# Kernel optimization log

Measured on AMD Instinct MI355X. Metric: run time of the kernel, lower is better.

Reference implementation:

```python
import jax, jax.numpy as jnp
import numpy as np

B, D, H, NG = 8192, 2048, 2048, 7  # batch, input_size, hidden_size, num gate networks


def setup_inputs() -> dict:
    key = jax.random.key(0)
    ks = jax.random.split(key, 7)
    hx = jax.random.normal(ks[0], (B, D), dtype=jnp.float32)
    cx1 = jax.random.normal(ks[1], (B, H), dtype=jnp.float32)
    cx2 = jax.random.normal(ks[2], (B, H), dtype=jnp.float32)
    tj = jax.random.uniform(ks[3], (B, 1), dtype=jnp.float32)
    dt = jax.random.uniform(ks[4], (B, 1), dtype=jnp.float32)
    # fused weights for the 7 gate/decay networks, order: i1,i2,f1,f2,o,z,d
    W = jax.random.normal(ks[5], (D, NG * H), dtype=jnp.float32) * (1.0 / np.sqrt(D))
    b = jax.random.normal(ks[6], (NG * H,), dtype=jnp.float32) * 0.01
    return {"hx": hx, "cx1": cx1, "cx2": cx2, "tj": tj, "dt": dt, "W": W, "b": b}


def reference(hx, cx1, cx2, tj, dt, W, b):
    # One fused GEMM for all 7 gate networks, then split.
    g = hx @ W + b  # [B, 7H]
    i1, i2, f1, f2, o, z_raw, d_raw = [g[:, k * H:(k + 1) * H] for k in range(NG)]
    sig = jax.nn.sigmoid
    i1, i2, f1, f2, o = sig(i1), sig(i2), sig(f1), sig(f2), sig(o)
    z = jnp.tanh(z_raw)                 # Tanh(LC_z(hx)) as in forward
    decay = jax.nn.softplus(d_raw)      # Decay_network: positive decay coeff
    cy1 = f1 * cx1 + i1 * z             # fast cell state
    cy2 = f2 * cx2 + i2 * z             # asymptotic cell state
    t = tj + dt
    # continuous-time decay: c(t) = cy2 + (cy1 - cy2) * exp(-decay * (t - tj))
    c_t = cy2 + (cy1 - cy2) * jnp.exp(-decay * (t - tj))
    h_t = o * jnp.tanh(c_t)             # get_h(t)
    return jnp.stack([cy1, cy2, h_t])   # [3, B, H]
```

## Files before the change

kernel.cpp:

```cpp
#include <hip/hip_runtime.h>
#include <hip/hip_bf16.h>
#include <stdint.h>


#define B_SZ 8192
#define D_SZ 2048
#define H_SZ 2048
#define NG   7
#define NW   (NG * H_SZ)
#define BM   256
#define BN   32
#define BK   32
#define NKST (D_SZ / BK)
#define NBX  (B_SZ / BM)
#define NBY  (H_SZ / BN)

#define WB_BYTES   ((size_t)NBY * NKST * 14336)
#define HXB_OFF    WB_BYTES
#define HXB_BYTES  ((size_t)NBX * NKST * 16384)
#define WS_NEEDED  (WB_BYTES + HXB_BYTES)

typedef __attribute__((ext_vector_type(8))) short bf16x8;
typedef __attribute__((ext_vector_type(4))) float f32x4;

__device__ __forceinline__ uint32_t cvtpk(float lo, float hi) {
    uint32_t r;
    asm("v_cvt_pk_bf16_f32 %0, %1, %2" : "=v"(r) : "v"(lo), "v"(hi));
    return r;
}
__device__ __forceinline__ void glds16(const void* g, void* l) {
    __builtin_amdgcn_global_load_lds(
        (const __attribute__((address_space(1))) uint32_t*)g,
        (__attribute__((address_space(3))) uint32_t*)l, 16, 0, 0);
}
__device__ __forceinline__ float sigmoidf_(float x) {
    return 1.0f / (1.0f + __expf(-x));
}
__device__ __forceinline__ float tanhf_(float x) {
    float ax = fabsf(x);
    float e = __expf(2.0f * ax);
    float t = 1.0f - 2.0f / (e + 1.0f);
    return copysignf(t, x);
}
__device__ __forceinline__ float softplusf_(float x) {
    return (x > 30.0f) ? x : __logf(1.0f + __expf(x));
}

__global__ __launch_bounds__(896) void conv_w(const float* __restrict__ W,
                                              char* __restrict__ wb)
{
    const int by = blockIdx.x >> 6;
    const int ks = blockIdx.x & 63;
    const int u  = threadIdx.x;
    const int r  = u >> 2;
    const int pc = u & 3;
    const int koct = pc ^ ((r >> 1) & 3);
    const int g  = r >> 5;
    const int n  = r & 31;
    const int col = g * H_SZ + by * BN + n;
    const float* src = W + (size_t)(ks * BK + koct * 8) * NW + col;
    float w0 = src[0];
    float w1 = src[(size_t)NW];
    float w2 = src[(size_t)2 * NW];
    float w3 = src[(size_t)3 * NW];
    float w4 = src[(size_t)4 * NW];
    float w5 = src[(size_t)5 * NW];
    float w6 = src[(size_t)6 * NW];
    float w7 = src[(size_t)7 * NW];
    uint4 o;
    o.x = cvtpk(w0, w1); o.y = cvtpk(w2, w3);
    o.z = cvtpk(w4, w5); o.w = cvtpk(w6, w7);
    *(uint4*)(wb + (size_t)blockIdx.x * 14336 + u * 16) = o;
}

__global__ __launch_bounds__(1024) void conv_hx(const float* __restrict__ hx,
                                                char* __restrict__ hxb)
{
    const int bx = blockIdx.x >> 6;
    const int ks = blockIdx.x & 63;
    const int u  = threadIdx.x;
    const int r  = u >> 2;
    const int pc = u & 3;
    const int koct = pc ^ ((r >> 1) & 3);
    const float* src = hx + (size_t)(bx * BM + r) * D_SZ + ks * BK + koct * 8;
    f32x4 a = *(const f32x4*)(src);
    f32x4 b = *(const f32x4*)(src + 4);
    uint4 o;
    o.x = cvtpk(a[0], a[1]); o.y = cvtpk(a[2], a[3]);
    o.z = cvtpk(b[0], b[1]); o.w = cvtpk(b[2], b[3]);
    *(uint4*)(hxb + (size_t)blockIdx.x * 16384 + u * 16) = o;
}

#define NTH3 512
#define BUFB 30720

#define SB0 __builtin_amdgcn_sched_barrier(0)

__global__ __launch_bounds__(NTH3, 2) void lstm_bf16(
    const char* __restrict__ wb, const char* __restrict__ hxb,
    const float* __restrict__ cx1, const float* __restrict__ cx2,
    const float* __restrict__ dt, const float* __restrict__ bias,
    float* __restrict__ out)
{
    __shared__ char smem[4 * BUFB];

    const int tid  = threadIdx.x;
    const int lane = tid & 63;
    const int wid  = tid >> 6;
    const int wm   = wid >> 1;
    const int wn   = wid & 1;
    const int l15  = lane & 15;
    const int lg   = lane >> 4;

    const int b0  = blockIdx.x;
    const int swz = (b0 & 7) * 256 + (b0 >> 3);
    const int by2 = swz >> 6;
    const int rem = swz & 63;
    const int bx  = rem >> 1;
    const int by  = by2 * 2 + (rem & 1);
    const int gm0 = bx * BM;
    const int n0  = by * BN;

    const int xch = (lg ^ ((l15 >> 1) & 3)) * 8;
    const uint32_t aAb = (uint32_t)(uintptr_t)smem + 2u * ((wm * 64 + l15) * 32 + xch);
    const uint32_t aBb = (uint32_t)(uintptr_t)smem + 16384u + 2u * ((wn * 16 + l15) * 32 + xch);
    const uint32_t aA0 = aAb,            aA1 = aAb + BUFB;
    const uint32_t aA2 = aAb + 2 * BUFB, aA3 = aAb + 3 * BUFB;
    const uint32_t aB0 = aBb,            aB1 = aBb + BUFB;
    const uint32_t aB2 = aBb + 2 * BUFB, aB3 = aBb + 3 * BUFB;

    const int lane16 = lane << 4;
    const char* hxp0 = hxb + (((size_t)(bx * NKST)) << 14) + (wid << 11) + lane16;
    const char* wbp0 = wb + (size_t)(by * NKST) * 14336 + wid * 1792 + lane16;
    char* dA0 = smem + (wid << 11);            char* dB0 = smem + 16384 + wid * 1792;
    char* dA1 = dA0 + BUFB;                    char* dB1 = dB0 + BUFB;
    char* dA2 = dA0 + 2 * BUFB;                char* dB2 = dB0 + 2 * BUFB;
    char* dA3 = dA0 + 3 * BUFB;                char* dB3 = dB0 + 3 * BUFB;

    f32x4 acc[NG][4];
    #pragma unroll
    for (int g = 0; g < NG; ++g)
        #pragma unroll
        for (int mf = 0; mf < 4; ++mf)
            acc[g][mf] = (f32x4){0.f, 0.f, 0.f, 0.f};

    bf16x8 fBE[NG], fBO[NG];
    bf16x8 fA0E, fA0O, fA1, fA2, fA3;

    #define ISSUE_A123(AAc) do {                                                   \
        asm volatile("ds_read_b128 %0, %1 offset:1024" : "=&v"(fA1) : "v"(AAc));   \
        asm volatile("ds_read_b128 %0, %1 offset:2048" : "=&v"(fA2) : "v"(AAc));   \
        asm volatile("ds_read_b128 %0, %1 offset:3072" : "=&v"(fA3) : "v"(AAc));   \
    } while (0)

    #define ISSUE_NEXT(ABn, AAn, FBN, FA0N) do {                                   \
        asm volatile("ds_read_b128 %0, %1"               : "=&v"(FBN[0]) : "v"(ABn)); \
        asm volatile("ds_read_b128 %0, %1 offset:2048"   : "=&v"(FBN[1]) : "v"(ABn)); \
        asm volatile("ds_read_b128 %0, %1 offset:4096"   : "=&v"(FBN[2]) : "v"(ABn)); \
        asm volatile("ds_read_b128 %0, %1 offset:6144"   : "=&v"(FBN[3]) : "v"(ABn)); \
        asm volatile("ds_read_b128 %0, %1 offset:8192"   : "=&v"(FBN[4]) : "v"(ABn)); \
        asm volatile("ds_read_b128 %0, %1 offset:10240"  : "=&v"(FBN[5]) : "v"(ABn)); \
        asm volatile("ds_read_b128 %0, %1 offset:12288"  : "=&v"(FBN[6]) : "v"(ABn)); \
        asm volatile("ds_read_b128 %0, %1"               : "=&v"(FA0N)   : "v"(AAn)); \
    } while (0)

    #define CLUSTER(FA, FBC, MF, LGN) do {                                         \
        asm volatile("s_waitcnt lgkmcnt(" #LGN ")" ::: "memory");                  \
        SB0;                                                                       \
        __builtin_amdgcn_s_setprio(1);                                             \
        _Pragma("unroll")                                                          \
        for (int g_ = 0; g_ < NG; ++g_)                                            \
            acc[g_][MF] = __builtin_amdgcn_mfma_f32_16x16x32_bf16(                 \
                FA, FBC[g_], acc[g_][MF], 0, 0, 0);                                \
        __builtin_amdgcn_s_setprio(0);                                             \
        SB0;                                                                       \
    } while (0)

    #define STAGE(SC) do {                                                         \
        glds16(hxp, dA##SC); glds16(hxp + 1024, dA##SC + 1024);                    \
        glds16(wbp, dB##SC);                                                       \
        if (lane < 48) glds16(wbp + 1024, dB##SC + 1024);                          \
        hxp += 16384; wbp += 14336;                                                \
    } while (0)

    #define STAGE_K(SC, K) do {                                                    \
        glds16(hxp0 + (K) * 16384, dA##SC);                                        \
        glds16(hxp0 + (K) * 16384 + 1024, dA##SC + 1024);                          \
        glds16(wbp0 + (K) * 14336, dB##SC);                                        \
        if (lane < 48) glds16(wbp0 + (K) * 14336 + 1024, dB##SC + 1024);           \
    } while (0)

    #define STEP_S(AAc, ABn, AAn, FBC, FBN, FA0C, FA0N, SC, VMN)  do {             \
        asm volatile("s_waitcnt vmcnt(" #VMN ")" ::: "memory");                    \
        __builtin_amdgcn_s_barrier();                                              \
        SB0;                                                                       \
        ISSUE_A123(AAc);                                                           \
        ISSUE_NEXT(ABn, AAn, FBN, FA0N);                                           \
        SB0;                                                                       \
        STAGE(SC);                                                                 \
        SB0;                                                                       \
        CLUSTER(FA0C, FBC, 0, 11);                                                 \
        CLUSTER(fA1,  FBC, 1, 10);                                                 \
        CLUSTER(fA2,  FBC, 2, 9);                                                  \
        CLUSTER(fA3,  FBC, 3, 8);                                                  \
    } while (0)

    #define STEP_N(AAc, ABn, AAn, FBC, FBN, FA0C, FA0N, VMN)  do {                 \
        asm volatile("s_waitcnt vmcnt(" #VMN ")" ::: "memory");                    \
        __builtin_amdgcn_s_barrier();                                              \
        SB0;                                                                       \
        ISSUE_A123(AAc);                                                           \
        ISSUE_NEXT(ABn, AAn, FBN, FA0N);                                           \
        SB0;                                                                       \
        CLUSTER(FA0C, FBC, 0, 11);                                                 \
        CLUSTER(fA1,  FBC, 1, 10);                                                 \
        CLUSTER(fA2,  FBC, 2, 9);                                                  \
        CLUSTER(fA3,  FBC, 3, 8);                                                  \
    } while (0)

    STAGE_K(0, 0);
    STAGE_K(1, 1);
    STAGE_K(2, 2);
    const char* hxp = hxp0 + 3 * 16384;
    const char* wbp = wbp0 + 3 * 14336;
    asm volatile("s_waitcnt vmcnt(8)" ::: "memory");
    __builtin_amdgcn_s_barrier();
    SB0;
    ISSUE_NEXT(aB0, aA0, fBE, fA0E);
    SB0;

    #pragma unroll 1
    for (int it = 0; it < 15; ++it) {
        STEP_S(aA0, aB1, aA1, fBE, fBO, fA0E, fA0O, 3, 4);
        STEP_S(aA1, aB2, aA2, fBO, fBE, fA0O, fA0E, 0, 4);
        STEP_S(aA2, aB3, aA3, fBE, fBO, fA0E, fA0O, 1, 4);
        STEP_S(aA3, aB0, aA0, fBO, fBE, fA0O, fA0E, 2, 4);
    }
    STEP_S(aA0, aB1, aA1, fBE, fBO, fA0E, fA0O, 3, 4);
    STEP_N(aA1, aB2, aA2, fBO, fBE, fA0O, fA0E, 4);
    STEP_N(aA2, aB3, aA3, fBE, fBO, fA0E, fA0O, 0);
    ISSUE_A123(aA3);
    SB0;
    CLUSTER(fA0O, fBO, 0, 3);
    CLUSTER(fA1,  fBO, 1, 2);
    CLUSTER(fA2,  fBO, 2, 1);
    CLUSTER(fA3,  fBO, 3, 0);

    const size_t BH = (size_t)B_SZ * H_SZ;
    const int j = n0 + wn * 16 + l15;
    float bj[NG];
    #pragma unroll
    for (int g = 0; g < NG; ++g) bj[g] = bias[g * H_SZ + j];

    #pragma unroll
    for (int mf = 0; mf < 4; ++mf) {
        #pragma unroll
        for (int r = 0; r < 4; ++r) {
            int row = gm0 + wm * 64 + mf * 16 + lg * 4 + r;
            float dtv = dt[row];
            float i1 = sigmoidf_(acc[0][mf][r] + bj[0]);
            float i2 = sigmoidf_(acc[1][mf][r] + bj[1]);
            float f1 = sigmoidf_(acc[2][mf][r] + bj[2]);
            float f2 = sigmoidf_(acc[3][mf][r] + bj[3]);
            float o  = sigmoidf_(acc[4][mf][r] + bj[4]);
            float z  = tanhf_(acc[5][mf][r] + bj[5]);
            float dec = softplusf_(acc[6][mf][r] + bj[6]);
            size_t idx = (size_t)row * H_SZ + j;
            float c1 = cx1[idx], c2 = cx2[idx];
            float cy1 = f1 * c1 + i1 * z;
            float cy2 = f2 * c2 + i2 * z;
            float ct  = cy2 + (cy1 - cy2) * __expf(-dec * dtv);
            float ht  = o * tanhf_(ct);
            out[idx]          = cy1;
            out[BH + idx]     = cy2;
            out[2 * BH + idx] = ht;
        }
    }
}

#define NTH  512
#define LDP  40
__global__ __launch_bounds__(NTH, 2) void lstm_f32(
    const float* __restrict__ hx, const float* __restrict__ cx1,
    const float* __restrict__ cx2, const float* __restrict__ dt,
    const float* __restrict__ W, const float* __restrict__ bias,
    float* __restrict__ out)
{
    __shared__ ushort sA[BM * LDP];
    __shared__ ushort sB[NG * BN * LDP];

    const int tid = threadIdx.x;
    const int nwg = gridDim.x;
    const int cpx = nwg >> 3;
    const int b0  = blockIdx.x;
    const int swz = (b0 & 7) * cpx + (b0 >> 3);
    const int bx  = swz & 31;
    const int by  = swz >> 5;
    const int gm0 = bx * BM;
    const int n0  = by * BN;

    const int lane = tid & 63;
    const int wid  = tid >> 6;
    const int wm   = wid >> 1;
    const int wn   = wid & 1;
    const int l15  = lane & 15;
    const int lg   = lane >> 4;

    const int ar0 = tid >> 2,          aq0 = tid & 3;
    const int ar1 = (tid + 512) >> 2,  aq1 = tid & 3;
    const bool hasB = (tid < 448);
    const int bg  = tid >> 6;
    const int bkq = (tid >> 3) & 7;
    const int bnq = tid & 7;

    f32x4 pa[4];
    f32x4 pb[4];

    auto issue_loads = [&](int K0) {
        {
            const float* p = hx + (size_t)(gm0 + ar0) * D_SZ + K0 + aq0 * 8;
            pa[0] = *(const f32x4*)(p);
            pa[1] = *(const f32x4*)(p + 4);
        }
        {
            const float* p = hx + (size_t)(gm0 + ar1) * D_SZ + K0 + aq1 * 8;
            pa[2] = *(const f32x4*)(p);
            pa[3] = *(const f32x4*)(p + 4);
        }
        if (hasB) {
            const float* p = W + (size_t)(K0 + bkq * 4) * NW + bg * H_SZ + n0 + bnq * 4;
            pb[0] = *(const f32x4*)(p);
            pb[1] = *(const f32x4*)(p + NW);
            pb[2] = *(const f32x4*)(p + 2 * NW);
            pb[3] = *(const f32x4*)(p + 3 * NW);
        }
    };

    auto store_lds = [&]() {
        {
            uint4 u;
            u.x = cvtpk(pa[0][0], pa[0][1]); u.y = cvtpk(pa[0][2], pa[0][3]);
            u.z = cvtpk(pa[1][0], pa[1][1]); u.w = cvtpk(pa[1][2], pa[1][3]);
            *(uint4*)(&sA[ar0 * LDP + aq0 * 8]) = u;
        }
        {
            uint4 u;
            u.x = cvtpk(pa[2][0], pa[2][1]); u.y = cvtpk(pa[2][2], pa[2][3]);
            u.z = cvtpk(pa[3][0], pa[3][1]); u.w = cvtpk(pa[3][2], pa[3][3]);
            *(uint4*)(&sA[ar1 * LDP + aq1 * 8]) = u;
        }
        if (hasB) {
            #pragma unroll
            for (int jj = 0; jj < 4; ++jj) {
                uint2 v;
                v.x = cvtpk(pb[0][jj], pb[1][jj]);
                v.y = cvtpk(pb[2][jj], pb[3][jj]);
                *(uint2*)(&sB[(bg * BN + bnq * 4 + jj) * LDP + bkq * 4]) = v;
            }
        }
    };

    f32x4 acc[NG][4];
    #pragma unroll
    for (int g = 0; g < NG; ++g)
        #pragma unroll
        for (int mf = 0; mf < 4; ++mf)
            acc[g][mf] = (f32x4){0.f, 0.f, 0.f, 0.f};

    int aoff[4];
    #pragma unroll
    for (int mf = 0; mf < 4; ++mf)
        aoff[mf] = (wm * 64 + mf * 16 + l15) * LDP + lg * 8;
    int boff[NG];
    #pragma unroll
    for (int g = 0; g < NG; ++g)
        boff[g] = (g * BN + wn * 16 + l15) * LDP + lg * 8;

    issue_loads(0);
    for (int kk = 0; kk < NKST; ++kk) {
        store_lds();
        __syncthreads();
        if (kk + 1 < NKST) issue_loads((kk + 1) * BK);

        bf16x8 af[4];
        #pragma unroll
        for (int mf = 0; mf < 4; ++mf)
            af[mf] = *(const bf16x8*)(&sA[aoff[mf]]);
        #pragma unroll
        for (int g = 0; g < NG; ++g) {
            bf16x8 bfr = *(const bf16x8*)(&sB[boff[g]]);
            #pragma unroll
            for (int mf = 0; mf < 4; ++mf)
                acc[g][mf] = __builtin_amdgcn_mfma_f32_16x16x32_bf16(
                    af[mf], bfr, acc[g][mf], 0, 0, 0);
        }
        __syncthreads();
    }

    const size_t BH = (size_t)B_SZ * H_SZ;
    const int j = n0 + wn * 16 + l15;
    float bj[NG];
    #pragma unroll
    for (int g = 0; g < NG; ++g) bj[g] = bias[g * H_SZ + j];

    #pragma unroll
    for (int mf = 0; mf < 4; ++mf) {
        #pragma unroll
        for (int r = 0; r < 4; ++r) {
            int row = gm0 + wm * 64 + mf * 16 + lg * 4 + r;
            float dtv = dt[row];
            float i1 = sigmoidf_(acc[0][mf][r] + bj[0]);
            float i2 = sigmoidf_(acc[1][mf][r] + bj[1]);
            float f1 = sigmoidf_(acc[2][mf][r] + bj[2]);
            float f2 = sigmoidf_(acc[3][mf][r] + bj[3]);
            float o  = sigmoidf_(acc[4][mf][r] + bj[4]);
            float z  = tanhf_(acc[5][mf][r] + bj[5]);
            float dec = softplusf_(acc[6][mf][r] + bj[6]);
            size_t idx = (size_t)row * H_SZ + j;
            float c1 = cx1[idx], c2 = cx2[idx];
            float cy1 = f1 * c1 + i1 * z;
            float cy2 = f2 * c2 + i2 * z;
            float ct  = cy2 + (cy1 - cy2) * __expf(-dec * dtv);
            float ht  = o * tanhf_(ct);
            out[idx]          = cy1;
            out[BH + idx]     = cy2;
            out[2 * BH + idx] = ht;
        }
    }
}

extern "C" void kernel_launch(void* const* d_in, const int* in_sizes, int n_in,
                              void* d_out, int out_size, void* d_ws, size_t ws_size,
                              hipStream_t stream) {
    const float* hx  = (const float*)d_in[0];
    const float* cx1 = (const float*)d_in[1];
    const float* cx2 = (const float*)d_in[2];
    const float* dt  = (const float*)d_in[4];
    const float* W   = (const float*)d_in[5];
    const float* b   = (const float*)d_in[6];
    float* out = (float*)d_out;

    if (ws_size >= WS_NEEDED) {
        char* wb  = (char*)d_ws;
        char* hxb = (char*)d_ws + HXB_OFF;
        conv_w<<<dim3(NBY * NKST), dim3(896), 0, stream>>>(W, wb);
        conv_hx<<<dim3(NBX * NKST), dim3(1024), 0, stream>>>(hx, hxb);
        lstm_bf16<<<dim3(NBX * NBY), dim3(NTH3), 0, stream>>>(
            wb, hxb, cx1, cx2, dt, b, out);
    } else {
        lstm_f32<<<dim3(NBX * NBY), dim3(NTH), 0, stream>>>(
            hx, cx1, cx2, dt, W, b, out);
    }
}
```

Baseline: 533.8 us.

## Replace double-buffered fragment prefetch with barrier-interleaved per-cluster schedule

Drops the even/odd register double-buffering of the A and B fragments, where the next k-step's LDS reads were issued ahead of the current MFMA clusters. Each k-step now reads its B fragments and one A fragment, then alternates a block barrier plus lgkmcnt(0) wait with one 7-MFMA cluster, spreading the global-to-LDS staging loads across the four clusters. The aim is to cut register pressure and keep the waves in lockstep so LDS reads and MFMAs ping-pong between them. The cost is four extra barriers per k-step, and LDS reads are no longer overlapped within a single wave.

```diff
diff --git a/kernel.cpp b/kernel.cpp
--- a/kernel.cpp
+++ b/kernel.cpp
@@ -144,78 +144,79 @@
         for (int mf = 0; mf < 4; ++mf)
             acc[g][mf] = (f32x4){0.f, 0.f, 0.f, 0.f};
 
-    bf16x8 fBE[NG], fBO[NG];
-    bf16x8 fA0E, fA0O, fA1, fA2, fA3;
-
-    #define ISSUE_A123(AAc) do {                                                   \
-        asm volatile("ds_read_b128 %0, %1 offset:1024" : "=&v"(fA1) : "v"(AAc));   \
-        asm volatile("ds_read_b128 %0, %1 offset:2048" : "=&v"(fA2) : "v"(AAc));   \
-        asm volatile("ds_read_b128 %0, %1 offset:3072" : "=&v"(fA3) : "v"(AAc));   \
-    } while (0)
-
-    #define ISSUE_NEXT(ABn, AAn, FBN, FA0N) do {                                   \
-        asm volatile("ds_read_b128 %0, %1"               : "=&v"(FBN[0]) : "v"(ABn)); \
-        asm volatile("ds_read_b128 %0, %1 offset:2048"   : "=&v"(FBN[1]) : "v"(ABn)); \
-        asm volatile("ds_read_b128 %0, %1 offset:4096"   : "=&v"(FBN[2]) : "v"(ABn)); \
-        asm volatile("ds_read_b128 %0, %1 offset:6144"   : "=&v"(FBN[3]) : "v"(ABn)); \
-        asm volatile("ds_read_b128 %0, %1 offset:8192"   : "=&v"(FBN[4]) : "v"(ABn)); \
-        asm volatile("ds_read_b128 %0, %1 offset:10240"  : "=&v"(FBN[5]) : "v"(ABn)); \
-        asm volatile("ds_read_b128 %0, %1 offset:12288"  : "=&v"(FBN[6]) : "v"(ABn)); \
-        asm volatile("ds_read_b128 %0, %1"               : "=&v"(FA0N)   : "v"(AAn)); \
-    } while (0)
-
-    #define CLUSTER(FA, FBC, MF, LGN) do {                                         \
-        asm volatile("s_waitcnt lgkmcnt(" #LGN ")" ::: "memory");                  \
-        SB0;                                                                       \
-        __builtin_amdgcn_s_setprio(1);                                             \
-        _Pragma("unroll")                                                          \
-        for (int g_ = 0; g_ < NG; ++g_)                                            \
-            acc[g_][MF] = __builtin_amdgcn_mfma_f32_16x16x32_bf16(                 \
-                FA, FBC[g_], acc[g_][MF], 0, 0, 0);                                \
-        __builtin_amdgcn_s_setprio(0);                                             \
-        SB0;                                                                       \
-    } while (0)
-
-    #define STAGE(SC) do {                                                         \
-        glds16(hxp, dA##SC); glds16(hxp + 1024, dA##SC + 1024);                    \
-        glds16(wbp, dB##SC);                                                       \
-        if (lane < 48) glds16(wbp + 1024, dB##SC + 1024);                          \
-        hxp += 16384; wbp += 14336;                                                \
-    } while (0)
-
-    #define STAGE_K(SC, K) do {                                                    \
-        glds16(hxp0 + (K) * 16384, dA##SC);                                        \
-        glds16(hxp0 + (K) * 16384 + 1024, dA##SC + 1024);                          \
-        glds16(wbp0 + (K) * 14336, dB##SC);                                        \
-        if (lane < 48) glds16(wbp0 + (K) * 14336 + 1024, dB##SC + 1024);           \
-    } while (0)
-
-    #define STEP_S(AAc, ABn, AAn, FBC, FBN, FA0C, FA0N, SC, VMN)  do {             \
-        asm volatile("s_waitcnt vmcnt(" #VMN ")" ::: "memory");                    \
-        __builtin_amdgcn_s_barrier();                                              \
-        SB0;                                                                       \
-        ISSUE_A123(AAc);                                                           \
-        ISSUE_NEXT(ABn, AAn, FBN, FA0N);                                           \
-        SB0;                                                                       \
-        STAGE(SC);                                                                 \
-        SB0;                                                                       \
-        CLUSTER(FA0C, FBC, 0, 11);                                                 \
-        CLUSTER(fA1,  FBC, 1, 10);                                                 \
-        CLUSTER(fA2,  FBC, 2, 9);                                                  \
-        CLUSTER(fA3,  FBC, 3, 8);                                                  \
-    } while (0)
-
-    #define STEP_N(AAc, ABn, AAn, FBC, FBN, FA0C, FA0N, VMN)  do {                 \
-        asm volatile("s_waitcnt vmcnt(" #VMN ")" ::: "memory");                    \
-        __builtin_amdgcn_s_barrier();                                              \
-        SB0;                                                                       \
-        ISSUE_A123(AAc);                                                           \
-        ISSUE_NEXT(ABn, AAn, FBN, FA0N);                                           \
-        SB0;                                                                       \
-        CLUSTER(FA0C, FBC, 0, 11);                                                 \
-        CLUSTER(fA1,  FBC, 1, 10);                                                 \
-        CLUSTER(fA2,  FBC, 2, 9);                                                  \
-        CLUSTER(fA3,  FBC, 3, 8);                                                  \
+    bf16x8 fB[NG];
+    bf16x8 fA0, fA1, fA2, fA3;
+
+    #define CL7(FA, MF) do {                                                   \
+        __builtin_amdgcn_s_setprio(1);                                         \
+        _Pragma("unroll")                                                      \
+        for (int g_ = 0; g_ < NG; ++g_)                                        \
+            acc[g_][MF] = __builtin_amdgcn_mfma_f32_16x16x32_bf16(             \
+                FA, fB[g_], acc[g_][MF], 0, 0, 0);                             \
+        __builtin_amdgcn_s_setprio(0);                                         \
+        SB0;                                                                   \
+    } while (0)
+
+    #define BARW do {                                                          \
+        __builtin_amdgcn_s_barrier();                                          \
+        asm volatile("s_waitcnt lgkmcnt(0)" ::: "memory");                     \
+        SB0;                                                                   \
+    } while (0)
+
+    #define RD_B(ABc) do {                                                     \
+        asm volatile("ds_read_b128 %0, %1"              : "=v"(fB[0]) : "v"(ABc)); \
+        asm volatile("ds_read_b128 %0, %1 offset:2048"  : "=v"(fB[1]) : "v"(ABc)); \
+        asm volatile("ds_read_b128 %0, %1 offset:4096"  : "=v"(fB[2]) : "v"(ABc)); \
+        asm volatile("ds_read_b128 %0, %1 offset:6144"  : "=v"(fB[3]) : "v"(ABc)); \
+        asm volatile("ds_read_b128 %0, %1 offset:8192"  : "=v"(fB[4]) : "v"(ABc)); \
+        asm volatile("ds_read_b128 %0, %1 offset:10240" : "=v"(fB[5]) : "v"(ABc)); \
+        asm volatile("ds_read_b128 %0, %1 offset:12288" : "=v"(fB[6]) : "v"(ABc)); \
+    } while (0)
+
+    #define HSTEP_S(AAc, ABc, SC) do {                                         \
+        asm volatile("s_waitcnt vmcnt(4)" ::: "memory");                       \
+        __builtin_amdgcn_s_barrier();                                          \
+        SB0;                                                                   \
+                                                                  \
+        RD_B(ABc);                                                             \
+        asm volatile("ds_read_b128 %0, %1"              : "=v"(fA0) : "v"(AAc)); \
+        glds16(hxp, dA##SC);                                                   \
+        SB0; BARW; CL7(fA0, 0);                                                \
+                                                                  \
+        asm volatile("ds_read_b128 %0, %1 offset:1024"  : "=v"(fA1) : "v"(AAc)); \
+        glds16(hxp + 1024, dA##SC + 1024);                                     \
+        SB0; BARW; CL7(fA1, 1);                                                \
+                                                                  \
+        asm volatile("ds_read_b128 %0, %1 offset:2048"  : "=v"(fA2) : "v"(AAc)); \
+        glds16(wbp, dB##SC);                                                   \
+        SB0; BARW; CL7(fA2, 2);                                                \
+                                                                  \
+        asm volatile("ds_read_b128 %0, %1 offset:3072"  : "=v"(fA3) : "v"(AAc)); \
+        if (lane < 48) glds16(wbp + 1024, dB##SC + 1024);                      \
+        SB0; BARW; CL7(fA3, 3);                                                \
+        hxp += 16384; wbp += 14336;                                            \
+    } while (0)
+
+    #define HSTEP_N(AAc, ABc, VMN) do {                                        \
+        asm volatile("s_waitcnt vmcnt(" #VMN ")" ::: "memory");                \
+        __builtin_amdgcn_s_barrier();                                          \
+        SB0;                                                                   \
+        RD_B(ABc);                                                             \
+        asm volatile("ds_read_b128 %0, %1"              : "=v"(fA0) : "v"(AAc)); \
+        SB0; BARW; CL7(fA0, 0);                                                \
+        asm volatile("ds_read_b128 %0, %1 offset:1024"  : "=v"(fA1) : "v"(AAc)); \
+        SB0; BARW; CL7(fA1, 1);                                                \
+        asm volatile("ds_read_b128 %0, %1 offset:2048"  : "=v"(fA2) : "v"(AAc)); \
+        SB0; BARW; CL7(fA2, 2);                                                \
+        asm volatile("ds_read_b128 %0, %1 offset:3072"  : "=v"(fA3) : "v"(AAc)); \
+        SB0; BARW; CL7(fA3, 3);                                                \
+    } while (0)
+
+    #define STAGE_K(SC, K) do {                                                \
+        glds16(hxp0 + (K) * 16384, dA##SC);                                    \
+        glds16(hxp0 + (K) * 16384 + 1024, dA##SC + 1024);                      \
+        glds16(wbp0 + (K) * 14336, dB##SC);                                    \
+        if (lane < 48) glds16(wbp0 + (K) * 14336 + 1024, dB##SC + 1024);       \
     } while (0)
 
     STAGE_K(0, 0);
@@ -223,28 +224,21 @@
     STAGE_K(2, 2);
     const char* hxp = hxp0 + 3 * 16384;
     const char* wbp = wbp0 + 3 * 14336;
-    asm volatile("s_waitcnt vmcnt(8)" ::: "memory");
+    asm volatile("s_waitcnt vmcnt(4)" ::: "memory");
     __builtin_amdgcn_s_barrier();
     SB0;
-    ISSUE_NEXT(aB0, aA0, fBE, fA0E);
-    SB0;
 
     #pragma unroll 1
     for (int it = 0; it < 15; ++it) {
-        STEP_S(aA0, aB1, aA1, fBE, fBO, fA0E, fA0O, 3, 4);
-        STEP_S(aA1, aB2, aA2, fBO, fBE, fA0O, fA0E, 0, 4);
-        STEP_S(aA2, aB3, aA3, fBE, fBO, fA0E, fA0O, 1, 4);
-        STEP_S(aA3, aB0, aA0, fBO, fBE, fA0O, fA0E, 2, 4);
+        HSTEP_S(aA0, aB0, 3);
+        HSTEP_S(aA1, aB1, 0);
+        HSTEP_S(aA2, aB2, 1);
+        HSTEP_S(aA3, aB3, 2);
     }
-    STEP_S(aA0, aB1, aA1, fBE, fBO, fA0E, fA0O, 3, 4);
-    STEP_N(aA1, aB2, aA2, fBO, fBE, fA0O, fA0E, 4);
-    STEP_N(aA2, aB3, aA3, fBE, fBO, fA0E, fA0O, 0);
-    ISSUE_A123(aA3);
-    SB0;
-    CLUSTER(fA0O, fBO, 0, 3);
-    CLUSTER(fA1,  fBO, 1, 2);
-    CLUSTER(fA2,  fBO, 2, 1);
-    CLUSTER(fA3,  fBO, 3, 0);
+    HSTEP_S(aA0, aB0, 3);
+    HSTEP_N(aA1, aB1, 4);
+    HSTEP_N(aA2, aB2, 4);
+    HSTEP_N(aA3, aB3, 0);
 
     const size_t BH = (size_t)B_SZ * H_SZ;
     const int j = n0 + wn * 16 + l15;
```

After: 544.9 us. 1.02x slower.
